# Kernel optimization log

Measured on AMD Instinct MI355X. Metric: run time of the kernel, lower is better.

The kernel has to match this reference:

```python
import jax, jax.numpy as jnp
import numpy as np

MAX_DIST = 5
D_PE = 16
NUM_ENTITIES = 50000
NUM_EDGES = 800000
NUM_ANCHOR_TRIPLES = 32
MAX_SOURCES = 2 * NUM_ANCHOR_TRIPLES  # upper bound on unique anchor entities


def setup_inputs() -> dict:
    key = jax.random.key(0)
    k1, k2, k3, k4 = jax.random.split(key, 4)
    h_ids = jax.random.randint(k1, (NUM_EDGES,), 0, NUM_ENTITIES)
    t_ids = jax.random.randint(k2, (NUM_EDGES,), 0, NUM_ENTITIES)
    anchor_triple_indices = jax.random.randint(k3, (NUM_ANCHOR_TRIPLES,), 0, NUM_EDGES)
    dist_embed = jax.random.normal(k4, (MAX_DIST + 1, D_PE), dtype=jnp.float32)
    return {
        "h_ids": h_ids,
        "t_ids": t_ids,
        "anchor_triple_indices": anchor_triple_indices,
        "num_entities": NUM_ENTITIES,
        "dist_embed": dist_embed,
    }


def _bfs_mean_counts(h_ids, t_ids, anchor_triple_indices, num_entities):
    """Returns [num_entities, MAX_DIST+1] mean one-hot distance counts over anchors."""
    # unique anchor entities, padded with -1 to a static size (torch.unique equivalent)
    anchor_ents = jnp.concatenate([h_ids[anchor_triple_indices], t_ids[anchor_triple_indices]])
    sources = jnp.unique(anchor_ents, size=MAX_SOURCES, fill_value=-1)  # [K], sorted
    valid = sources >= 0                                                # [K]
    src = jnp.where(valid, sources, 0)
    K = src.shape[0]
    col = jnp.arange(K)

    # symmetric adjacency as edge list (duplicates are harmless: only >0 is tested)
    edge_src = jnp.concatenate([h_ids, t_ids])  # [2E]
    edge_dst = jnp.concatenate([t_ids, h_ids])  # [2E]

    frontier = jnp.zeros((num_entities, K), jnp.float32).at[src, col].set(1.0)
    visited = jnp.zeros((num_entities, K), bool).at[src, col].set(True)
    dist = jnp.full((num_entities, K), MAX_DIST, jnp.int32).at[src, col].set(0)

    for depth in range(1, MAX_DIST + 1):  # fixed small hop count
        # sparse adj @ frontier == scatter-add of gathered frontier rows
        new_frontier = jax.ops.segment_sum(frontier[edge_src], edge_dst, num_segments=num_entities)
        newly = (new_frontier > 0) & ~visited
        dist = jnp.where(newly, depth, dist)
        visited = visited | newly
        frontier = newly.astype(jnp.float32)

    # masked mean over valid anchor sources, expressed as distance-count histogram
    w = valid.astype(jnp.float32)
    n_valid = jnp.maximum(w.sum(), 1.0)
    onehot = jax.nn.one_hot(dist, MAX_DIST + 1, dtype=jnp.float32)  # [N, K, D+1]
    counts = jnp.einsum('nkd,k->nd', onehot, w) / n_valid           # [N, D+1]
    return counts


def reference(h_ids, t_ids, anchor_triple_indices, num_entities, dist_embed):
    counts = _bfs_mean_counts(h_ids, t_ids, anchor_triple_indices, num_entities)
    # mean over sources of embed(dist) == counts @ embedding table
    return counts @ dist_embed  # [num_entities, d_pe]
```

## Files before the change

kernel.cpp:

```cpp
#include <hip/hip_runtime.h>
#include <hip/hip_bf16.h>

typedef unsigned long long u64;
typedef unsigned int u32;
typedef unsigned short u16;

#define MAXD 5
#define BSH  6
#define BN   64
#define NW   512
#define NTH  256
#define NBMAX 1024
#define CAPG 2816
#define HEMPTY 0xFFFFFFFFu


__global__ __launch_bounds__(NTH) void chunk_sort(
    const int* __restrict__ h, const int* __restrict__ t, int E, int CE, int CAPC,
    int NB, u32* __restrict__ recs, u16* __restrict__ segtab,
    const int* __restrict__ anchor, int A,
    u64* __restrict__ NFg, u32* __restrict__ srcPack, int* __restrict__ nvalid) {
    extern __shared__ u32 sh[];
    u32* s     = sh;
    u32* cur   = sh + NBMAX;
    u32* hsKey = cur + NB;
    u32* hsBit = hsKey + 128;
    u32* buf   = hsBit + 128;
    int tid = threadIdx.x, c = blockIdx.x;
    int lo = c * CE, hi = min(E, lo + CE);
    int nrec = 2 * (hi - lo);

    for (int i = tid; i < NB; i += NTH) cur[i] = 0u;
    if (tid < 128) hsKey[tid] = HEMPTY;
    __syncthreads();

    if (tid < 64) {
        int K = 2 * A;
        int a_ = (tid < K) ? anchor[(tid < A) ? tid : (tid - A)] : 0;
        int my = (tid < K) ? ((tid < A) ? h[a_] : t[a_]) : -1;
        bool uniq = (tid < K);
        for (int j = 0; j < 64; ++j) {
            int o = __shfl(my, j, 64);
            if (j < tid && o == my) uniq = false;
        }
        u64 mask = __ballot(uniq);
        if (c == 0 && tid == 0) *nvalid = (int)__popcll(mask);
        if (uniq) {
            u32 slot = ((u32)my * 2654435761u) >> 25;
            while (atomicCAS(&hsKey[slot], HEMPTY, (u32)my) != HEMPTY)
                slot = (slot + 1) & 127u;
            hsBit[slot] = (u32)tid;
        }
        if (c == 0)
            srcPack[tid] = uniq ? (((u32)my << BSH) | (u32)tid) : HEMPTY;
    }
    __syncthreads();

    for (int e = lo + tid; e < hi; e += NTH) {
        u32 uu = (u32)h[e], vv = (u32)t[e];
        atomicAdd(&cur[vv >> BSH], 1u);
        atomicAdd(&cur[uu >> BSH], 1u);
    }
    __syncthreads();

    for (int k = 0; k < NBMAX / NTH; ++k) {
        int i = tid + NTH * k;
        s[i] = (i < NB) ? cur[i] : 0u;
    }
    __syncthreads();
    for (int d = 1; d < NBMAX; d <<= 1) {
        u32 v0[NBMAX / NTH];
#pragma unroll
        for (int k = 0; k < NBMAX / NTH; ++k) {
            int i = tid + NTH * k;
            v0[k] = (i >= d) ? s[i - d] : 0u;
        }
        __syncthreads();
#pragma unroll
        for (int k = 0; k < NBMAX / NTH; ++k) s[tid + NTH * k] += v0[k];
        __syncthreads();
    }
    for (int i = tid; i < NB; i += NTH) {
        u32 excl = s[i] - cur[i];
        s[i] = excl;
        cur[i] = 0u;
        segtab[c * (NB + 1) + i] = (u16)excl;
    }
    if (tid == 0) segtab[c * (NB + 1) + NB] = (u16)nrec;
    __syncthreads();

    auto srcMask = [&](u32 src) -> u64 {
        u32 slot = (src * 2654435761u) >> 25;
        while (true) {
            u32 k = hsKey[slot];
            if (k == src) return 1ull << hsBit[slot];
            if (k == HEMPTY) return 0ull;
            slot = (slot + 1) & 127u;
        }
    };

    for (int e = lo + tid; e < hi; e += NTH) {
        u32 uu = (u32)h[e], vv = (u32)t[e];
        u32 b1 = vv >> BSH;
        buf[s[b1] + atomicAdd(&cur[b1], 1u)] = (uu << BSH) | (vv & (BN - 1));
        u32 b2 = uu >> BSH;
        buf[s[b2] + atomicAdd(&cur[b2], 1u)] = (vv << BSH) | (uu & (BN - 1));
        if (uu != vv) {
            u64 m1 = srcMask(uu);
            if (m1) atomicOr(&NFg[vv], m1);
            u64 m2 = srcMask(vv);
            if (m2) atomicOr(&NFg[uu], m2);
        }
    }
    __syncthreads();
    for (int i = tid; i < nrec; i += NTH) recs[c * CAPC + i] = buf[i];
}

__global__ __launch_bounds__(NTH) void level12_merge(
    const u32* __restrict__ recs, const u16* __restrict__ segtab, int CAPC, int NB,
    const u32* __restrict__ srcPack, const u64* __restrict__ NFg,
    u64* __restrict__ F2, u64* __restrict__ V, u64* __restrict__ CNT,
    u32* __restrict__ recs2, u32* __restrict__ bucketCnt, int N) {
    __shared__ u32 s0[NW];
    __shared__ u32 loff[NW + 1];
    __shared__ u64 NF[BN];
    __shared__ u32 srcL[64];
    int b = blockIdx.x, tid = threadIdx.x;
    if (tid < BN) NF[tid] = 0ull;
    if (tid < 64) srcL[tid] = srcPack[tid];
    for (int c = tid; c < NW; c += NTH) {
        const u16* st = segtab + c * (NB + 1);
        u32 a = st[b], e = st[b + 1];
        s0[c] = a;
        loff[c] = e - a;
    }
    __syncthreads();
    for (int d = 1; d < NW; d <<= 1) {
        u32 v0[NW / NTH];
#pragma unroll
        for (int k = 0; k < NW / NTH; ++k) {
            int i = tid + NTH * k;
            v0[k] = (i >= d) ? loff[i - d] : 0u;
        }
        __syncthreads();
#pragma unroll
        for (int k = 0; k < NW / NTH; ++k) loff[tid + NTH * k] += v0[k];
        __syncthreads();
    }
    u32 T;
    {
        if (tid == 0) T = loff[NW - 1];
        u32 tmp[NW / NTH];
#pragma unroll
        for (int k = 0; k < NW / NTH; ++k) {
            int i = tid + NTH * k;
            tmp[k] = (i == 0) ? 0u : loff[i - 1];
        }
        __syncthreads();
#pragma unroll
        for (int k = 0; k < NW / NTH; ++k) {
            int i = tid + NTH * k;
            if (i == 0) {  }
        }
        if (tid == 0) loff[NW] = loff[NW - 1];
        __syncthreads();
#pragma unroll
        for (int k = 0; k < NW / NTH; ++k) loff[tid + NTH * k] = tmp[k];
        __syncthreads();
        T = loff[NW];
    }
    u32 o0 = (u32)b * CAPG;

    auto fetch = [&](u32 j) -> u32 {
        int c = 0;
#pragma unroll
        for (int step = 256; step >= 1; step >>= 1)
            if (c + step <= NW - 1 && loff[c + step] <= j) c += step;
        u32 rec = recs[(u32)c * CAPC + s0[c] + (j - loff[c])];
        if (j < (u32)CAPG) recs2[o0 + j] = rec;
        return rec;
    };

    u32 j = tid;
    for (; j + 3u * NTH < T; j += 4u * NTH) {
        u32 r0 = fetch(j), r1 = fetch(j + NTH);
        u32 r2 = fetch(j + 2 * NTH), r3 = fetch(j + 3 * NTH);
        u64 f0 = NFg[r0 >> BSH], f1 = NFg[r1 >> BSH];
        u64 f2 = NFg[r2 >> BSH], f3 = NFg[r3 >> BSH];
        if (f0) atomicOr(&NF[r0 & (BN - 1)], f0);
        if (f1) atomicOr(&NF[r1 & (BN - 1)], f1);
        if (f2) atomicOr(&NF[r2 & (BN - 1)], f2);
        if (f3) atomicOr(&NF[r3 & (BN - 1)], f3);
    }
    for (; j < T; j += NTH) {
        u32 r0 = fetch(j);
        u64 f0 = NFg[r0 >> BSH];
        if (f0) atomicOr(&NF[r0 & (BN - 1)], f0);
    }
    __syncthreads();
    if (tid == 0) bucketCnt[b] = min(T, (u32)CAPG);
    if (tid < BN) {
        int n = b * BN + tid;
        if (n < N) {
            u64 srcbit = 0ull;
            for (int k = 0; k < 64; ++k) {
                u32 p = srcL[k];
                if (p != HEMPTY && (int)(p >> BSH) == n)
                    srcbit |= 1ull << (p & (BN - 1));
            }
            u64 nf1 = NFg[n];
            u64 v1 = srcbit | nf1;
            u64 newly2 = NF[tid] & ~v1;
            V[n] = v1 | newly2;
            F2[n] = newly2;
            CNT[n] = (srcbit ? 1ull : 0ull)
                   | ((u64)__popcll(nf1) << 8)
                   | ((u64)__popcll(newly2) << 16);
        }
    }
}

__global__ __launch_bounds__(NTH) void level3(
    const u32* __restrict__ recs2, const u32* __restrict__ bucketCnt,
    const u64* __restrict__ Fin, u64* __restrict__ Fout,
    u64* __restrict__ V, u64* __restrict__ CNT, int N) {
    __shared__ u64 NF[BN];
    int b = blockIdx.x, tid = threadIdx.x;
    u32 o0 = (u32)b * CAPG;
    u32 cnt = bucketCnt[b];
    if (tid < BN) NF[tid] = 0ull;
    __syncthreads();
    u32 r = tid;
    for (; r + 3u * NTH < cnt; r += 4u * NTH) {
        u32 c0 = recs2[o0 + r],           c1 = recs2[o0 + r + NTH];
        u32 c2 = recs2[o0 + r + 2 * NTH], c3 = recs2[o0 + r + 3 * NTH];
        u64 f0 = Fin[c0 >> BSH], f1 = Fin[c1 >> BSH];
        u64 f2 = Fin[c2 >> BSH], f3 = Fin[c3 >> BSH];
        if (f0) atomicOr(&NF[c0 & (BN - 1)], f0);
        if (f1) atomicOr(&NF[c1 & (BN - 1)], f1);
        if (f2) atomicOr(&NF[c2 & (BN - 1)], f2);
        if (f3) atomicOr(&NF[c3 & (BN - 1)], f3);
    }
    for (; r < cnt; r += NTH) {
        u32 c0 = recs2[o0 + r];
        u64 f0 = Fin[c0 >> BSH];
        if (f0) atomicOr(&NF[c0 & (BN - 1)], f0);
    }
    __syncthreads();
    if (tid < BN) {
        int n = b * BN + tid;
        if (n < N) {
            u64 vis = V[n];
            u64 newly = NF[tid] & ~vis;
            Fout[n] = newly;
            if (newly) {
                V[n] = vis | newly;
                CNT[n] += (u64)__popcll(newly) << 24;
            }
        }
    }
}

__global__ __launch_bounds__(NTH) void level4_fin(
    const u32* __restrict__ recs2, const u32* __restrict__ bucketCnt,
    const u64* __restrict__ Fin, const u64* __restrict__ V,
    const u64* __restrict__ CNT, const int* __restrict__ nvalid,
    const float* __restrict__ embed, float* __restrict__ out, int N) {
    __shared__ u64 NF[BN];
    int b = blockIdx.x, tid = threadIdx.x;
    u32 o0 = (u32)b * CAPG;
    u32 cnt = bucketCnt[b];
    if (tid < BN) NF[tid] = 0ull;
    __syncthreads();
    u32 r = tid;
    for (; r + 3u * NTH < cnt; r += 4u * NTH) {
        u32 c0 = recs2[o0 + r],           c1 = recs2[o0 + r + NTH];
        u32 c2 = recs2[o0 + r + 2 * NTH], c3 = recs2[o0 + r + 3 * NTH];
        u64 f0 = Fin[c0 >> BSH], f1 = Fin[c1 >> BSH];
        u64 f2 = Fin[c2 >> BSH], f3 = Fin[c3 >> BSH];
        if (f0) atomicOr(&NF[c0 & (BN - 1)], f0);
        if (f1) atomicOr(&NF[c1 & (BN - 1)], f1);
        if (f2) atomicOr(&NF[c2 & (BN - 1)], f2);
        if (f3) atomicOr(&NF[c3 & (BN - 1)], f3);
    }
    for (; r < cnt; r += NTH) {
        u32 c0 = recs2[o0 + r];
        u64 f0 = Fin[c0 >> BSH];
        if (f0) atomicOr(&NF[c0 & (BN - 1)], f0);
    }
    __syncthreads();
    int nl = tid >> 2, q = tid & 3;
    int n = b * BN + nl;
    if (n >= N) return;
    u64 vis = V[n];
    int c4 = __popcll(NF[nl] & ~vis);
    u64 c = CNT[n];
    int nv = *nvalid;
    float inv = 1.0f / (float)(nv > 0 ? nv : 1);
    float cd[MAXD + 1];
    int total = c4;
#pragma unroll
    for (int d = 0; d < 4; ++d) {
        int x = (int)((c >> (8 * d)) & 0xffull);
        total += x;
        cd[d] = (float)x;
    }
    cd[4] = (float)c4;
    cd[5] = (float)(nv - total);

    const float4* e4 = (const float4*)embed;
    float4 acc = {0.f, 0.f, 0.f, 0.f};
#pragma unroll
    for (int d = 0; d <= MAXD; ++d) {
        float4 e = e4[d * 4 + q];
        acc.x += cd[d] * e.x; acc.y += cd[d] * e.y;
        acc.z += cd[d] * e.z; acc.w += cd[d] * e.w;
    }
    acc.x *= inv; acc.y *= inv; acc.z *= inv; acc.w *= inv;
    ((float4*)(out + (size_t)n * 16))[q] = acc;
}

extern "C" void kernel_launch(void* const* d_in, const int* in_sizes, int n_in,
                              void* d_out, int out_size, void* d_ws, size_t ws_size,
                              hipStream_t stream) {
    const int*   h      = (const int*)d_in[0];
    const int*   t      = (const int*)d_in[1];
    const int*   anchor = (const int*)d_in[2];
    const float* embed  = (const float*)d_in[4];
    float*       out    = (float*)d_out;

    int E = in_sizes[0];
    int A = in_sizes[2];
    int D = in_sizes[4] / (MAXD + 1);
    int N = out_size / D;
    int NB = (N + BN - 1) >> BSH;
    int CE = (E + NW - 1) / NW;
    int CAPC = 2 * CE;
    (void)D;

    u64* NFg = (u64*)d_ws;
    u64* V   = NFg + N;
    u64* CNT = V + N;
    u64* F2  = CNT + N;
    u64* F3  = F2 + N;
    u32* srcPack   = (u32*)(F3 + N);
    int* nvalid    = (int*)(srcPack + 64);
    u32* bucketCnt = (u32*)(nvalid + 1);
    u32* recs      = bucketCnt + NB;
    u16* segtab    = (u16*)(recs + (size_t)NW * CAPC);
    u32* recs2     = (u32*)(segtab + (size_t)NW * (NB + 1));

    hipMemsetAsync(NFg, 0, (size_t)N * 8, stream);

    size_t shmem = (size_t)(NBMAX + NB + 256 + CAPC) * sizeof(u32);
    chunk_sort<<<NW, NTH, shmem, stream>>>(h, t, E, CE, CAPC, NB, recs, segtab,
                                           anchor, A, NFg, srcPack, nvalid);

    level12_merge<<<NB, NTH, 0, stream>>>(recs, segtab, CAPC, NB, srcPack, NFg,
                                          F2, V, CNT, recs2, bucketCnt, N);
    level3<<<NB, NTH, 0, stream>>>(recs2, bucketCnt, F2, F3, V, CNT, N);
    level4_fin<<<NB, NTH, 0, stream>>>(recs2, bucketCnt, F3, V, CNT,
                                       nvalid, embed, out, N);
}
```

Baseline: 138.8 us.

## Stage edges in LDS, use wave-shuffle scans, and gather merge records contiguously

chunk_sort now loads each chunk's (h,t) pairs into shared memory once, so the counting and scatter passes no longer re-read global memory. The Hillis-Steele block scans with many barriers in chunk_sort and level12_merge become wave-level shuffle scans plus a small per-wave offset sum. level12_merge now gathers its bucket's records into an LDS buffer. Each thread takes a contiguous range and walks the chunk index linearly instead of doing a binary search per element, and the buffer is then read for coalesced writes and the NF updates. This trades larger LDS use (which may lower occupancy) for fewer global loads and fewer syncs.

```diff
diff --git a/kernel.cpp b/kernel.cpp
--- a/kernel.cpp
+++ b/kernel.cpp
@@ -10,7 +10,6 @@
 #define BN   64
 #define NW   512
 #define NTH  256
-#define NBMAX 1024
 #define CAPG 2816
 #define HEMPTY 0xFFFFFFFFu
 
@@ -20,16 +19,22 @@
     int NB, u32* __restrict__ recs, u16* __restrict__ segtab,
     const int* __restrict__ anchor, int A,
     u64* __restrict__ NFg, u32* __restrict__ srcPack, int* __restrict__ nvalid) {
-    extern __shared__ u32 sh[];
-    u32* s     = sh;
-    u32* cur   = sh + NBMAX;
+    extern __shared__ u64 dyn[];
+    u64* edl   = dyn;
+    u32* buf   = (u32*)(edl + CE);
+    u32* offs  = buf + CAPC;
+    u32* cur   = offs + NB;
     u32* hsKey = cur + NB;
     u32* hsBit = hsKey + 128;
-    u32* buf   = hsBit + 128;
+    u32* waveSum = hsBit + 128;
     int tid = threadIdx.x, c = blockIdx.x;
+    int lane = tid & 63, w = tid >> 6;
     int lo = c * CE, hi = min(E, lo + CE);
-    int nrec = 2 * (hi - lo);
-
+    int ne = hi - lo;
+    int nrec = 2 * ne;
+
+    for (int i = tid; i < ne; i += NTH)
+        edl[i] = ((u64)(u32)h[lo + i] << 32) | (u32)t[lo + i];
     for (int i = tid; i < NB; i += NTH) cur[i] = 0u;
     if (tid < 128) hsKey[tid] = HEMPTY;
     __syncthreads();
@@ -54,39 +59,49 @@
         if (c == 0)
             srcPack[tid] = uniq ? (((u32)my << BSH) | (u32)tid) : HEMPTY;
     }
-    __syncthreads();
-
-    for (int e = lo + tid; e < hi; e += NTH) {
-        u32 uu = (u32)h[e], vv = (u32)t[e];
+
+    for (int i = tid; i < ne; i += NTH) {
+        u64 e = edl[i];
+        u32 uu = (u32)(e >> 32), vv = (u32)e;
         atomicAdd(&cur[vv >> BSH], 1u);
         atomicAdd(&cur[uu >> BSH], 1u);
     }
     __syncthreads();
 
-    for (int k = 0; k < NBMAX / NTH; ++k) {
-        int i = tid + NTH * k;
-        s[i] = (i < NB) ? cur[i] : 0u;
-    }
-    __syncthreads();
-    for (int d = 1; d < NBMAX; d <<= 1) {
-        u32 v0[NBMAX / NTH];
-#pragma unroll
-        for (int k = 0; k < NBMAX / NTH; ++k) {
-            int i = tid + NTH * k;
-            v0[k] = (i >= d) ? s[i - d] : 0u;
-        }
+    {
+        u32 i0 = (u32)tid * 4;
+        u32 aa[4];
+#pragma unroll
+        for (int k = 0; k < 4; ++k) {
+            u32 i = i0 + k;
+            aa[k] = (i < (u32)NB) ? cur[i] : 0u;
+        }
+        u32 sum = aa[0] + aa[1] + aa[2] + aa[3];
+        u32 p = sum;
+#pragma unroll
+        for (int d = 1; d < 64; d <<= 1) {
+            u32 x = (u32)__shfl_up((int)p, d, 64);
+            if (lane >= d) p += x;
+        }
+        u32 excl = p - sum;
+        if (lane == 63) waveSum[w] = p;
         __syncthreads();
-#pragma unroll
-        for (int k = 0; k < NBMAX / NTH; ++k) s[tid + NTH * k] += v0[k];
-        __syncthreads();
-    }
-    for (int i = tid; i < NB; i += NTH) {
-        u32 excl = s[i] - cur[i];
-        s[i] = excl;
-        cur[i] = 0u;
-        segtab[c * (NB + 1) + i] = (u16)excl;
-    }
-    if (tid == 0) segtab[c * (NB + 1) + NB] = (u16)nrec;
+        u32 woff = 0;
+        for (int k = 0; k < w; ++k) woff += waveSum[k];
+        u32 o0 = woff + excl;
+        u32 o1 = o0 + aa[0], o2 = o1 + aa[1], o3 = o2 + aa[2];
+        u32 oo[4] = {o0, o1, o2, o3};
+#pragma unroll
+        for (int k = 0; k < 4; ++k) {
+            u32 i = i0 + k;
+            if (i < (u32)NB) {
+                offs[i] = oo[k];
+                segtab[c * (NB + 1) + i] = (u16)oo[k];
+                cur[i] = 0u;
+            }
+        }
+        if (tid == 0) segtab[c * (NB + 1) + NB] = (u16)nrec;
+    }
     __syncthreads();
 
     auto srcMask = [&](u32 src) -> u64 {
@@ -99,12 +114,13 @@
         }
     };
 
-    for (int e = lo + tid; e < hi; e += NTH) {
-        u32 uu = (u32)h[e], vv = (u32)t[e];
+    for (int i = tid; i < ne; i += NTH) {
+        u64 e = edl[i];
+        u32 uu = (u32)(e >> 32), vv = (u32)e;
         u32 b1 = vv >> BSH;
-        buf[s[b1] + atomicAdd(&cur[b1], 1u)] = (uu << BSH) | (vv & (BN - 1));
+        buf[offs[b1] + atomicAdd(&cur[b1], 1u)] = (uu << BSH) | (vv & (BN - 1));
         u32 b2 = uu >> BSH;
-        buf[s[b2] + atomicAdd(&cur[b2], 1u)] = (vv << BSH) | (uu & (BN - 1));
+        buf[offs[b2] + atomicAdd(&cur[b2], 1u)] = (vv << BSH) | (uu & (BN - 1));
         if (uu != vv) {
             u64 m1 = srcMask(uu);
             if (m1) atomicOr(&NFg[vv], m1);
@@ -121,70 +137,66 @@
     const u32* __restrict__ srcPack, const u64* __restrict__ NFg,
     u64* __restrict__ F2, u64* __restrict__ V, u64* __restrict__ CNT,
     u32* __restrict__ recs2, u32* __restrict__ bucketCnt, int N) {
-    __shared__ u32 s0[NW];
+    __shared__ u32 s0a[NW];
     __shared__ u32 loff[NW + 1];
+    __shared__ u32 waveSum[4];
+    __shared__ u32 buf[CAPG];
     __shared__ u64 NF[BN];
     __shared__ u32 srcL[64];
     int b = blockIdx.x, tid = threadIdx.x;
+    int lane = tid & 63, w = tid >> 6;
     if (tid < BN) NF[tid] = 0ull;
     if (tid < 64) srcL[tid] = srcPack[tid];
-    for (int c = tid; c < NW; c += NTH) {
-        const u16* st = segtab + c * (NB + 1);
-        u32 a = st[b], e = st[b + 1];
-        s0[c] = a;
-        loff[c] = e - a;
-    }
-    __syncthreads();
-    for (int d = 1; d < NW; d <<= 1) {
-        u32 v0[NW / NTH];
-#pragma unroll
-        for (int k = 0; k < NW / NTH; ++k) {
-            int i = tid + NTH * k;
-            v0[k] = (i >= d) ? loff[i - d] : 0u;
-        }
-        __syncthreads();
-#pragma unroll
-        for (int k = 0; k < NW / NTH; ++k) loff[tid + NTH * k] += v0[k];
-        __syncthreads();
-    }
-    u32 T;
-    {
-        if (tid == 0) T = loff[NW - 1];
-        u32 tmp[NW / NTH];
-#pragma unroll
-        for (int k = 0; k < NW / NTH; ++k) {
-            int i = tid + NTH * k;
-            tmp[k] = (i == 0) ? 0u : loff[i - 1];
-        }
-        __syncthreads();
-#pragma unroll
-        for (int k = 0; k < NW / NTH; ++k) {
-            int i = tid + NTH * k;
-            if (i == 0) {  }
-        }
-        if (tid == 0) loff[NW] = loff[NW - 1];
-        __syncthreads();
-#pragma unroll
-        for (int k = 0; k < NW / NTH; ++k) loff[tid + NTH * k] = tmp[k];
-        __syncthreads();
-        T = loff[NW];
-    }
+
+    u32 c0 = 2 * tid, c1 = 2 * tid + 1;
+    u32 a0 = segtab[c0 * (NB + 1) + b], e0 = segtab[c0 * (NB + 1) + b + 1];
+    u32 a1 = segtab[c1 * (NB + 1) + b], e1 = segtab[c1 * (NB + 1) + b + 1];
+    s0a[c0] = a0;
+    s0a[c1] = a1;
+    u32 l0 = e0 - a0, l1 = e1 - a1;
+    u32 sum = l0 + l1;
+    u32 p = sum;
+#pragma unroll
+    for (int d = 1; d < 64; d <<= 1) {
+        u32 x = (u32)__shfl_up((int)p, d, 64);
+        if (lane >= d) p += x;
+    }
+    u32 excl = p - sum;
+    if (lane == 63) waveSum[w] = p;
+    __syncthreads();
+    u32 woff = 0;
+    for (int k = 0; k < w; ++k) woff += waveSum[k];
+    u32 base = woff + excl;
+    loff[c0] = base;
+    loff[c1] = base + l0;
+    if (tid == NTH - 1) loff[NW] = base + l0 + l1;
+    __syncthreads();
+
+    u32 T = min(loff[NW], (u32)CAPG);
+
+    u32 per = (T + NTH - 1) / NTH;
+    u32 j0 = min((u32)tid * per, T), j1 = min(j0 + per, T);
+    if (j0 < j1) {
+        int c = 0;
+#pragma unroll
+        for (int step = 256; step >= 1; step >>= 1)
+            if (c + step <= NW - 1 && loff[c + step] <= j0) c += step;
+        for (u32 j = j0; j < j1; ++j) {
+            while (loff[c + 1] <= j) ++c;
+            buf[j] = recs[(u32)c * CAPC + s0a[c] + (j - loff[c])];
+        }
+    }
+    __syncthreads();
+
     u32 o0 = (u32)b * CAPG;
-
-    auto fetch = [&](u32 j) -> u32 {
-        int c = 0;
-#pragma unroll
-        for (int step = 256; step >= 1; step >>= 1)
-            if (c + step <= NW - 1 && loff[c + step] <= j) c += step;
-        u32 rec = recs[(u32)c * CAPC + s0[c] + (j - loff[c])];
-        if (j < (u32)CAPG) recs2[o0 + j] = rec;
-        return rec;
-    };
-
-    u32 j = tid;
-    for (; j + 3u * NTH < T; j += 4u * NTH) {
-        u32 r0 = fetch(j), r1 = fetch(j + NTH);
-        u32 r2 = fetch(j + 2 * NTH), r3 = fetch(j + 3 * NTH);
+    u32 r = tid;
+    for (; r + 3u * NTH < T; r += 4u * NTH) {
+        u32 r0 = buf[r],           r1 = buf[r + NTH];
+        u32 r2 = buf[r + 2 * NTH], r3 = buf[r + 3 * NTH];
+        recs2[o0 + r] = r0;
+        recs2[o0 + r + NTH] = r1;
+        recs2[o0 + r + 2 * NTH] = r2;
+        recs2[o0 + r + 3 * NTH] = r3;
         u64 f0 = NFg[r0 >> BSH], f1 = NFg[r1 >> BSH];
         u64 f2 = NFg[r2 >> BSH], f3 = NFg[r3 >> BSH];
         if (f0) atomicOr(&NF[r0 & (BN - 1)], f0);
@@ -192,21 +204,22 @@
         if (f2) atomicOr(&NF[r2 & (BN - 1)], f2);
         if (f3) atomicOr(&NF[r3 & (BN - 1)], f3);
     }
-    for (; j < T; j += NTH) {
-        u32 r0 = fetch(j);
+    for (; r < T; r += NTH) {
+        u32 r0 = buf[r];
+        recs2[o0 + r] = r0;
         u64 f0 = NFg[r0 >> BSH];
         if (f0) atomicOr(&NF[r0 & (BN - 1)], f0);
     }
     __syncthreads();
-    if (tid == 0) bucketCnt[b] = min(T, (u32)CAPG);
+    if (tid == 0) bucketCnt[b] = T;
     if (tid < BN) {
         int n = b * BN + tid;
         if (n < N) {
             u64 srcbit = 0ull;
             for (int k = 0; k < 64; ++k) {
-                u32 p = srcL[k];
-                if (p != HEMPTY && (int)(p >> BSH) == n)
-                    srcbit |= 1ull << (p & (BN - 1));
+                u32 pk = srcL[k];
+                if (pk != HEMPTY && (int)(pk >> BSH) == n)
+                    srcbit |= 1ull << (pk & (BN - 1));
             }
             u64 nf1 = NFg[n];
             u64 v1 = srcbit | nf1;
@@ -352,7 +365,8 @@
 
     hipMemsetAsync(NFg, 0, (size_t)N * 8, stream);
 
-    size_t shmem = (size_t)(NBMAX + NB + 256 + CAPC) * sizeof(u32);
+    size_t shmem = (size_t)CE * 8
+                 + (size_t)(CAPC + NB + NB + 128 + 128 + 4) * sizeof(u32);
     chunk_sort<<<NW, NTH, shmem, stream>>>(h, t, E, CE, CAPC, NB, recs, segtab,
                                            anchor, A, NFg, srcPack, nvalid);
 
```

New measurement: 138.0 us. No clear change (-0.6%).
